# Performance work log

Measured on AMD Instinct MI355X. Metric: run time of the kernel, lower is better.

Reference implementation:

```python
import jax, jax.numpy as jnp
import numpy as np

N, K, G, E, OUT = 50000, 32, 512, 400000, 8
EPS = 1e-8


def setup_inputs() -> dict:
    key = jax.random.key(0)
    ks = jax.random.split(key, 9)
    X = jax.random.uniform(ks[0], (N, G), dtype=jnp.float32)          # counts-like, non-negative
    Mu = jax.random.uniform(ks[1], (K, G), dtype=jnp.float32)
    Var = jax.random.uniform(ks[2], (K, G), dtype=jnp.float32) + 0.5  # keep variances bounded away from 0
    edge_index = jax.random.randint(ks[3], (2, E), 0, N)
    # learned parameters
    W = jax.random.normal(ks[4], (N, K), dtype=jnp.float32) * 0.1     # module inits zeros; small randn for non-trivial grads
    S = jnp.ones((N, 1), jnp.float32)
    glorot = float(np.sqrt(6.0 / (G + OUT)))
    Wl = jax.random.uniform(ks[5], (G, OUT), jnp.float32, -glorot, glorot)
    bl = jnp.zeros((OUT,), jnp.float32)
    Wr = jax.random.uniform(ks[6], (G, OUT), jnp.float32, -glorot, glorot)
    br = jnp.zeros((OUT,), jnp.float32)
    att = jax.random.normal(ks[7], (OUT,), jnp.float32) * 0.3
    return dict(X=X, Mu=Mu, Var=Var, W=W, S=S, Wl=Wl, bl=bl, Wr=Wr, br=br, att=att, edge_index=edge_index)


def reference(X, Mu, Var, W, S, Wl, bl, Wr, br, att, edge_index):
    P = jax.nn.softmax(W, axis=1)                                     # [N,K]

    # Gaussian NLL term: F[n,k] = -0.5 * sum_g (X[n,g] - Mu[k,g]*S[n])^2 / Var[k,g]
    # expanded into three GEMM-shaped contractions to avoid the [N,K,G] intermediate
    inv_var = 1.0 / Var                                               # [K,G]
    q1 = (X * X) @ inv_var.T                                          # [N,K]
    q2 = X @ (Mu * inv_var).T                                         # [N,K]
    q3 = jnp.sum(Mu * Mu * inv_var, axis=1)                           # [K]
    s = S[:, 0]                                                       # [N]
    Fmat = -0.5 * (q1 - 2.0 * s[:, None] * q2 + (s * s)[:, None] * q3[None, :])
    ll_prot = jnp.sum(P * Fmat) / X.shape[0]

    # GATv2 attention (heads=1, out=8, no self loops): only alpha is consumed downstream
    src, dst = edge_index[0], edge_index[1]
    xl = X @ Wl + bl                                                  # source transform [N,8]
    xr = X @ Wr + br                                                  # target transform [N,8]
    e = jax.nn.leaky_relu(xl[src] + xr[dst], 0.2) @ att               # [E]
    # segment softmax over edges grouped by destination node
    m = jax.lax.stop_gradient(jax.ops.segment_max(e, dst, num_segments=N))
    ex = jnp.exp(e - m[dst])
    denom = jax.ops.segment_sum(ex, dst, num_segments=N)
    alpha = ex / denom[dst]                                           # [E]

    ce_space = -jnp.sum(P[src] * alpha[:, None] * jnp.log(P[dst] + EPS)) / X.shape[0]
    return ll_prot, ce_space, P
```

## Files before the change

### kernel.cpp

```cpp
#include <hip/hip_runtime.h>
#include <hip/hip_bf16.h>
#include <math.h>

#define N_NODES 50000
#define K_COMP  32
#define G_DIM   512
#define E_EDGES 400000
#define OUT_DIM 8
#define EPSV    1e-8f

#define NPB 16
#define NB_NODE (N_NODES / NPB)
#define NB_E1   ((E_EDGES + 255) / 256)
#define NB_CE   ((E_EDGES / 2 + 255) / 256)

typedef __attribute__((ext_vector_type(8))) short short8;
typedef __attribute__((ext_vector_type(8))) unsigned short ushort8;
typedef __attribute__((ext_vector_type(4))) unsigned short ushort4v;
typedef __attribute__((ext_vector_type(4))) float f32x4;

static const size_t OFF_T     = 0;
static const size_t OFF_Q3    = OFF_T + 80 * 512;
static const size_t OFF_XL    = OFF_Q3 + 64;
static const size_t OFF_XR    = OFF_XL + (size_t)N_NODES * 8;
static const size_t OFF_PC    = OFF_XR + (size_t)N_NODES * 8;
static const size_t OFF_LOGP  = OFF_PC + (size_t)N_NODES * 32;
static const size_t OFF_CON   = OFF_LOGP + (size_t)N_NODES * 32;
static const size_t OFF_DENOM = OFF_CON + E_EDGES;
static const size_t OFF_PLL   = OFF_DENOM + N_NODES;
static const size_t OFF_PCE   = OFF_PLL + 4096;

__device__ __forceinline__ unsigned short f2bf(float f) {
    __hip_bfloat16 h = __float2bfloat16(f);
    return *(unsigned short*)&h;
}
__device__ __forceinline__ float bf2f(unsigned short u) {
    unsigned v = ((unsigned)u) << 16;
    return __uint_as_float(v);
}

__global__ __launch_bounds__(256)
void prep_kernel(const float* __restrict__ Var, const float* __restrict__ Mu,
                 const float* __restrict__ Wl, const float* __restrict__ Wr,
                 unsigned short* __restrict__ Tb, float* __restrict__ denom,
                 float* __restrict__ q3) {
    int idx = blockIdx.x * 256 + threadIdx.x;
    if (idx < 80 * 512) {
        int r = idx >> 9;
        int g = idx & 511;
        float v;
        if (r < 32)      v = 1.0f / Var[r * 512 + g];
        else if (r < 64) { int k = r - 32; v = Mu[k * 512 + g] / Var[k * 512 + g]; }
        else if (r < 72) { int o = r - 64; v = Wl[g * 8 + o]; }
        else             { int o = r - 72; v = Wr[g * 8 + o]; }
        int dest = ((g >> 5) * 5 + (r >> 4)) * 512 + (r & 15) * 32 + (((g & 31) >> 3) << 3) + (g & 7);
        Tb[dest] = f2bf(v);
    }
    if (idx < N_NODES) denom[idx] = 0.0f;

    if (blockIdx.x < 32) {
        int k = blockIdx.x;
        int t = threadIdx.x;
        float s = 0.0f;
        for (int g = t; g < 512; g += 256) {
            float mu = Mu[k * 512 + g];
            s += mu * mu / Var[k * 512 + g];
        }
        for (int off = 32; off; off >>= 1) s += __shfl_down(s, off);
        __shared__ float sQ[4];
        if ((t & 63) == 0) sQ[t >> 6] = s;
        __syncthreads();
        if (t == 0) q3[k] = sQ[0] + sQ[1] + sQ[2] + sQ[3];
    }
}

__global__ __launch_bounds__(128, 5)
void node_kernel(const float* __restrict__ X, const float* __restrict__ W,
                 const float* __restrict__ S, const float* __restrict__ bl,
                 const float* __restrict__ br, const unsigned short* __restrict__ Tb,
                 const float* __restrict__ q3, float* __restrict__ outP,
                 unsigned short* __restrict__ Pcb, unsigned short* __restrict__ logPb,
                 float* __restrict__ xl, float* __restrict__ xr,
                 float* __restrict__ pll) {
    __shared__ float sAccH[2][NPB][81];
    __shared__ float sLL[2];

    const int t = threadIdx.x;
    const int lane = t & 63;
    const int wv = t >> 6;
    const int col = lane & 15;
    const int kg  = lane >> 4;

    const int node = blockIdx.x * NPB + col;
    const float* xrow = X + (size_t)node * 512 + wv * 256 + kg * 8;

    f32x4 acc[5];
#pragma unroll
    for (int i = 0; i < 5; ++i) acc[i] = (f32x4){0.f, 0.f, 0.f, 0.f};

    float4 v0 = *(const float4*)(xrow);
    float4 v1 = *(const float4*)(xrow + 4);

#pragma unroll
    for (int gc = 0; gc < 256; gc += 32) {
        float4 n0v, n1v;
        if (gc + 32 < 256) {
            n0v = *(const float4*)(xrow + gc + 32);
            n1v = *(const float4*)(xrow + gc + 36);
        }
        const unsigned short* bbase =
            Tb + (size_t)(wv * 8 + (gc >> 5)) * 5 * 512 + col * 32 + kg * 8;
        short8 b0 = *(const short8*)(bbase);
        short8 b1 = *(const short8*)(bbase + 512);
        short8 b2 = *(const short8*)(bbase + 1024);
        short8 b3 = *(const short8*)(bbase + 1536);
        short8 b4 = *(const short8*)(bbase + 2048);

        short8 ax, ax2;
        ax[0] = (short)f2bf(v0.x); ax[1] = (short)f2bf(v0.y);
        ax[2] = (short)f2bf(v0.z); ax[3] = (short)f2bf(v0.w);
        ax[4] = (short)f2bf(v1.x); ax[5] = (short)f2bf(v1.y);
        ax[6] = (short)f2bf(v1.z); ax[7] = (short)f2bf(v1.w);
        ax2[0] = (short)f2bf(v0.x * v0.x); ax2[1] = (short)f2bf(v0.y * v0.y);
        ax2[2] = (short)f2bf(v0.z * v0.z); ax2[3] = (short)f2bf(v0.w * v0.w);
        ax2[4] = (short)f2bf(v1.x * v1.x); ax2[5] = (short)f2bf(v1.y * v1.y);
        ax2[6] = (short)f2bf(v1.z * v1.z); ax2[7] = (short)f2bf(v1.w * v1.w);

        acc[0] = __builtin_amdgcn_mfma_f32_16x16x32_bf16(ax2, b0, acc[0], 0, 0, 0);
        acc[1] = __builtin_amdgcn_mfma_f32_16x16x32_bf16(ax2, b1, acc[1], 0, 0, 0);
        acc[2] = __builtin_amdgcn_mfma_f32_16x16x32_bf16(ax,  b2, acc[2], 0, 0, 0);
        acc[3] = __builtin_amdgcn_mfma_f32_16x16x32_bf16(ax,  b3, acc[3], 0, 0, 0);
        acc[4] = __builtin_amdgcn_mfma_f32_16x16x32_bf16(ax,  b4, acc[4], 0, 0, 0);

        v0 = n0v; v1 = n1v;
    }

#pragma unroll
    for (int tile = 0; tile < 5; ++tile)
#pragma unroll
        for (int r = 0; r < 4; ++r)
            sAccH[wv][kg * 4 + r][tile * 16 + col] = acc[tile][r];
    __syncthreads();

    const int nn = t >> 3;
    const int j = t & 7;
    const int n = blockIdx.x * NPB + nn;

    float sv = S[n];
    float sv2 = sv * sv;
    float4 wv4 = *(const float4*)(W + (size_t)n * 32 + j * 4);
    float w[4] = {wv4.x, wv4.y, wv4.z, wv4.w};
    float wm = fmaxf(fmaxf(w[0], w[1]), fmaxf(w[2], w[3]));
    wm = fmaxf(wm, __shfl_xor(wm, 1));
    wm = fmaxf(wm, __shfl_xor(wm, 2));
    wm = fmaxf(wm, __shfl_xor(wm, 4));
    float p[4], ps = 0.0f;
#pragma unroll
    for (int i = 0; i < 4; ++i) { p[i] = __expf(w[i] - wm); ps += p[i]; }
    ps += __shfl_xor(ps, 1);
    ps += __shfl_xor(ps, 2);
    ps += __shfl_xor(ps, 4);
    float inv = 1.0f / ps;

    float pv[4];
    ushort4v pb, lb;
    float ll = 0.0f;
#pragma unroll
    for (int i = 0; i < 4; ++i) {
        int k = j * 4 + i;
        float P_ = p[i] * inv;
        pv[i] = P_;
        pb[i] = f2bf(P_);
        lb[i] = f2bf(__logf(P_ + EPSV));
        float q1k = sAccH[0][nn][k] + sAccH[1][nn][k];
        float q2k = sAccH[0][nn][32 + k] + sAccH[1][nn][32 + k];
        float f = -0.5f * (q1k - 2.0f * sv * q2k + sv2 * q3[k]);
        ll = fmaf(P_, f, ll);
    }
    ll += __shfl_xor(ll, 1);
    ll += __shfl_xor(ll, 2);
    ll += __shfl_xor(ll, 4);
    float llacc = (j == 0) ? ll : 0.0f;

    size_t base = (size_t)n * 32 + j * 4;
    float2* op = (float2*)(outP + base);
    op[0] = make_float2(pv[0], pv[1]);
    op[1] = make_float2(pv[2], pv[3]);
    *(ushort4v*)&Pcb[base] = pb;
    *(ushort4v*)&logPb[base] = lb;

    float xlv = (sAccH[0][nn][64 + j] + sAccH[1][nn][64 + j]) + bl[j];
    float xrv = (sAccH[0][nn][72 + j] + sAccH[1][nn][72 + j]) + br[j];
    xl[(size_t)n * 8 + j] = xlv;
    xr[(size_t)n * 8 + j] = xrv;

    for (int off = 32; off; off >>= 1) llacc += __shfl_down(llacc, off);
    if ((t & 63) == 0) sLL[wv] = llacc;
    __syncthreads();
    if (t == 0) pll[blockIdx.x] = sLL[0] + sLL[1];
}

__global__ __launch_bounds__(256, 4)
void edge1_kernel(const int* __restrict__ ei, const float* __restrict__ xl,
                  const float* __restrict__ xr, const float* __restrict__ att,
                  const unsigned short* __restrict__ Pcb,
                  const unsigned short* __restrict__ logPb,
                  float* __restrict__ contrib, float* __restrict__ denom) {
    int i = blockIdx.x * 256 + threadIdx.x;
    if (i >= E_EDGES) return;
    int s = ei[i];
    int d = ei[E_EDGES + i];
    const float4* ap = (const float4*)(xl + (size_t)s * 8);
    const float4* bp = (const float4*)(xr + (size_t)d * 8);
    const ushort8* pp = (const ushort8*)&Pcb[(size_t)s * 32];
    const ushort8* lp = (const ushort8*)&logPb[(size_t)d * 32];
    float4 a0 = ap[0], a1 = ap[1];
    float4 b0 = bp[0], b1 = bp[1];
    ushort8 pa = pp[0], pb_ = pp[1], pc = pp[2], pd = pp[3];
    ushort8 la = lp[0], lb_ = lp[1], lc = lp[2], ld = lp[3];
    const float4* atp = (const float4*)att;
    float4 t0 = atp[0], t1 = atp[1];
    float at[8] = {t0.x, t0.y, t0.z, t0.w, t1.x, t1.y, t1.z, t1.w};
    float h[8] = {a0.x + b0.x, a0.y + b0.y, a0.z + b0.z, a0.w + b0.w,
                  a1.x + b1.x, a1.y + b1.y, a1.z + b1.z, a1.w + b1.w};
    float ev = 0.0f;
#pragma unroll
    for (int q = 0; q < 8; ++q) {
        float hv = h[q];
        hv = hv > 0.0f ? hv : 0.2f * hv;
        ev = fmaf(hv, at[q], ev);
    }
    float x = __expf(ev);
    atomicAdd(denom + d, x);

    float dot = 0.0f;
#pragma unroll
    for (int r = 0; r < 8; ++r) {
        dot = fmaf(bf2f(pa[r]),  bf2f(la[r]),  dot);
        dot = fmaf(bf2f(pb_[r]), bf2f(lb_[r]), dot);
        dot = fmaf(bf2f(pc[r]),  bf2f(lc[r]),  dot);
        dot = fmaf(bf2f(pd[r]),  bf2f(ld[r]),  dot);
    }
    contrib[i] = x * dot;
}

__global__ __launch_bounds__(256, 4)
void edge2_kernel(const int* __restrict__ ei, const float* __restrict__ contrib,
                  const float* __restrict__ denom, float* __restrict__ pce) {
    const int t = threadIdx.x;
    const int base = (blockIdx.x * 256 + t) * 2;
    float ce = 0.0f;
    if (base < E_EDGES) {
        int2 dd = *(const int2*)&ei[E_EDGES + base];
        float2 cv = *(const float2*)&contrib[base];
        float den0 = denom[dd.x];
        float den1 = denom[dd.y];
        ce = cv.x / den0 + cv.y / den1;
    }
    for (int off = 32; off; off >>= 1) ce += __shfl_down(ce, off);
    __shared__ float sC[4];
    if ((t & 63) == 0) sC[t >> 6] = ce;
    __syncthreads();
    if (t == 0) pce[blockIdx.x] = sC[0] + sC[1] + sC[2] + sC[3];
}

__global__ __launch_bounds__(256)
void finalize_kernel(const float* __restrict__ pll, const float* __restrict__ pce,
                     float* __restrict__ out) {
    const int t = threadIdx.x;
    float a = 0.0f, b = 0.0f;
    for (int i = t; i < NB_NODE; i += 256) a += pll[i];
    for (int i = t; i < NB_CE; i += 256) b += pce[i];
    for (int off = 32; off; off >>= 1) {
        a += __shfl_down(a, off);
        b += __shfl_down(b, off);
    }
    __shared__ float sA[4], sB[4];
    if ((t & 63) == 0) { sA[t >> 6] = a; sB[t >> 6] = b; }
    __syncthreads();
    if (t == 0) {
        float ll = sA[0] + sA[1] + sA[2] + sA[3];
        float ce = sB[0] + sB[1] + sB[2] + sB[3];
        out[0] = ll / (float)N_NODES;
        out[1] = -ce / (float)N_NODES;
    }
}

extern "C" void kernel_launch(void* const* d_in, const int* in_sizes, int n_in,
                              void* d_out, int out_size, void* d_ws, size_t ws_size,
                              hipStream_t stream) {
    const float* X   = (const float*)d_in[0];
    const float* Mu  = (const float*)d_in[1];
    const float* Var = (const float*)d_in[2];
    const float* W   = (const float*)d_in[3];
    const float* S   = (const float*)d_in[4];
    const float* Wl  = (const float*)d_in[5];
    const float* bl  = (const float*)d_in[6];
    const float* Wr  = (const float*)d_in[7];
    const float* br  = (const float*)d_in[8];
    const float* att = (const float*)d_in[9];
    const int*   ei  = (const int*)d_in[10];
    float* out = (float*)d_out;
    float* ws  = (float*)d_ws;

    unsigned short* Tb      = (unsigned short*)(ws + OFF_T);
    float*          q3      = ws + OFF_Q3;
    float*          xl      = ws + OFF_XL;
    float*          xr      = ws + OFF_XR;
    unsigned short* Pcb     = (unsigned short*)(ws + OFF_PC);
    unsigned short* logPb   = (unsigned short*)(ws + OFF_LOGP);
    float*          contrib = ws + OFF_CON;
    float*          denom   = ws + OFF_DENOM;
    float*          pll     = ws + OFF_PLL;
    float*          pce     = ws + OFF_PCE;

    prep_kernel<<<(N_NODES + 255) / 256, 256, 0, stream>>>(Var, Mu, Wl, Wr, Tb, denom, q3);
    node_kernel<<<NB_NODE, 128, 0, stream>>>(X, W, S, bl, br, Tb, q3,
                                             out + 2, Pcb, logPb, xl, xr, pll);
    edge1_kernel<<<NB_E1, 256, 0, stream>>>(ei, xl, xr, att, Pcb, logPb, contrib, denom);
    edge2_kernel<<<NB_CE, 256, 0, stream>>>(ei, contrib, denom, pce);
    finalize_kernel<<<1, 256, 0, stream>>>(pll, pce, out);
}
```

Before: 80.94 us.

## Fold edge softmax normalization into per-destination atomics and pack node records

Because alpha normalizes by a per-destination denominator, the CE sum can be taken per destination as sum(x*dot)/sum(x). The edge kernel now atomically accumulates both quantities per node, and a small per-node kernel replaces the second pass over all edges and the per-edge contrib buffer. Per-node xl plus P and xr plus logP are also packed into contiguous 128-byte source and destination records, so each edge gathers one record per endpoint. The cost is a second atomic per edge and a larger zero-init in prep.

```diff
diff --git a/kernel.cpp b/kernel.cpp
--- a/kernel.cpp
+++ b/kernel.cpp
@@ -12,23 +12,21 @@
 #define NPB 16
 #define NB_NODE (N_NODES / NPB)
 #define NB_E1   ((E_EDGES + 255) / 256)
-#define NB_CE   ((E_EDGES / 2 + 255) / 256)
+#define NB_CEN  ((N_NODES + 255) / 256)
+#define NB_PREP ((2 * N_NODES + 255) / 256)
 
 typedef __attribute__((ext_vector_type(8))) short short8;
 typedef __attribute__((ext_vector_type(8))) unsigned short ushort8;
 typedef __attribute__((ext_vector_type(4))) unsigned short ushort4v;
 typedef __attribute__((ext_vector_type(4))) float f32x4;
 
-static const size_t OFF_T     = 0;
-static const size_t OFF_Q3    = OFF_T + 80 * 512;
-static const size_t OFF_XL    = OFF_Q3 + 64;
-static const size_t OFF_XR    = OFF_XL + (size_t)N_NODES * 8;
-static const size_t OFF_PC    = OFF_XR + (size_t)N_NODES * 8;
-static const size_t OFF_LOGP  = OFF_PC + (size_t)N_NODES * 32;
-static const size_t OFF_CON   = OFF_LOGP + (size_t)N_NODES * 32;
-static const size_t OFF_DENOM = OFF_CON + E_EDGES;
-static const size_t OFF_PLL   = OFF_DENOM + N_NODES;
-static const size_t OFF_PCE   = OFF_PLL + 4096;
+static const size_t OFF_T    = 0;
+static const size_t OFF_Q3   = OFF_T + 80 * 512;
+static const size_t OFF_SRC  = OFF_Q3 + 64;
+static const size_t OFF_DST  = OFF_SRC + (size_t)N_NODES * 32;
+static const size_t OFF_ND   = OFF_DST + (size_t)N_NODES * 32;
+static const size_t OFF_PLL  = OFF_ND + 2 * (size_t)N_NODES;
+static const size_t OFF_PCE  = OFF_PLL + 4096;
 
 __device__ __forceinline__ unsigned short f2bf(float f) {
     __hip_bfloat16 h = __float2bfloat16(f);
@@ -42,7 +40,7 @@
 __global__ __launch_bounds__(256)
 void prep_kernel(const float* __restrict__ Var, const float* __restrict__ Mu,
                  const float* __restrict__ Wl, const float* __restrict__ Wr,
-                 unsigned short* __restrict__ Tb, float* __restrict__ denom,
+                 unsigned short* __restrict__ Tb, float* __restrict__ nd,
                  float* __restrict__ q3) {
     int idx = blockIdx.x * 256 + threadIdx.x;
     if (idx < 80 * 512) {
@@ -56,7 +54,7 @@
         int dest = ((g >> 5) * 5 + (r >> 4)) * 512 + (r & 15) * 32 + (((g & 31) >> 3) << 3) + (g & 7);
         Tb[dest] = f2bf(v);
     }
-    if (idx < N_NODES) denom[idx] = 0.0f;
+    if (idx < 2 * N_NODES) nd[idx] = 0.0f;
 
     if (blockIdx.x < 32) {
         int k = blockIdx.x;
@@ -79,8 +77,7 @@
                  const float* __restrict__ S, const float* __restrict__ bl,
                  const float* __restrict__ br, const unsigned short* __restrict__ Tb,
                  const float* __restrict__ q3, float* __restrict__ outP,
-                 unsigned short* __restrict__ Pcb, unsigned short* __restrict__ logPb,
-                 float* __restrict__ xl, float* __restrict__ xr,
+                 float* __restrict__ srcRec, float* __restrict__ dstRec,
                  float* __restrict__ pll) {
     __shared__ float sAccH[2][NPB][81];
     __shared__ float sLL[2];
@@ -186,13 +183,13 @@
     float2* op = (float2*)(outP + base);
     op[0] = make_float2(pv[0], pv[1]);
     op[1] = make_float2(pv[2], pv[3]);
-    *(ushort4v*)&Pcb[base] = pb;
-    *(ushort4v*)&logPb[base] = lb;
-
-    float xlv = (sAccH[0][nn][64 + j] + sAccH[1][nn][64 + j]) + bl[j];
-    float xrv = (sAccH[0][nn][72 + j] + sAccH[1][nn][72 + j]) + br[j];
-    xl[(size_t)n * 8 + j] = xlv;
-    xr[(size_t)n * 8 + j] = xrv;
+
+    float* sr = srcRec + (size_t)n * 32;
+    float* dr = dstRec + (size_t)n * 32;
+    *(ushort4v*)&((unsigned short*)sr)[16 + j * 4] = pb;
+    *(ushort4v*)&((unsigned short*)dr)[16 + j * 4] = lb;
+    sr[j] = (sAccH[0][nn][64 + j] + sAccH[1][nn][64 + j]) + bl[j];
+    dr[j] = (sAccH[0][nn][72 + j] + sAccH[1][nn][72 + j]) + br[j];
 
     for (int off = 32; off; off >>= 1) llacc += __shfl_down(llacc, off);
     if ((t & 63) == 0) sLL[wv] = llacc;
@@ -201,21 +198,19 @@
 }
 
 __global__ __launch_bounds__(256, 4)
-void edge1_kernel(const int* __restrict__ ei, const float* __restrict__ xl,
-                  const float* __restrict__ xr, const float* __restrict__ att,
-                  const unsigned short* __restrict__ Pcb,
-                  const unsigned short* __restrict__ logPb,
-                  float* __restrict__ contrib, float* __restrict__ denom) {
+void edge1_kernel(const int* __restrict__ ei, const float* __restrict__ srcRec,
+                  const float* __restrict__ dstRec, const float* __restrict__ att,
+                  float* __restrict__ nd) {
     int i = blockIdx.x * 256 + threadIdx.x;
     if (i >= E_EDGES) return;
     int s = ei[i];
     int d = ei[E_EDGES + i];
-    const float4* ap = (const float4*)(xl + (size_t)s * 8);
-    const float4* bp = (const float4*)(xr + (size_t)d * 8);
-    const ushort8* pp = (const ushort8*)&Pcb[(size_t)s * 32];
-    const ushort8* lp = (const ushort8*)&logPb[(size_t)d * 32];
-    float4 a0 = ap[0], a1 = ap[1];
-    float4 b0 = bp[0], b1 = bp[1];
+    const float4* sp = (const float4*)(srcRec + (size_t)s * 32);
+    const float4* dp = (const float4*)(dstRec + (size_t)d * 32);
+    float4 a0 = sp[0], a1 = sp[1];
+    float4 b0 = dp[0], b1 = dp[1];
+    const ushort8* pp = (const ushort8*)(sp + 2);
+    const ushort8* lp = (const ushort8*)(dp + 2);
     ushort8 pa = pp[0], pb_ = pp[1], pc = pp[2], pd = pp[3];
     ushort8 la = lp[0], lb_ = lp[1], lc = lp[2], ld = lp[3];
     const float4* atp = (const float4*)att;
@@ -231,7 +226,6 @@
         ev = fmaf(hv, at[q], ev);
     }
     float x = __expf(ev);
-    atomicAdd(denom + d, x);
 
     float dot = 0.0f;
 #pragma unroll
@@ -241,21 +235,18 @@
         dot = fmaf(bf2f(pc[r]),  bf2f(lc[r]),  dot);
         dot = fmaf(bf2f(pd[r]),  bf2f(ld[r]),  dot);
     }
-    contrib[i] = x * dot;
-}
-
-__global__ __launch_bounds__(256, 4)
-void edge2_kernel(const int* __restrict__ ei, const float* __restrict__ contrib,
-                  const float* __restrict__ denom, float* __restrict__ pce) {
+    atomicAdd(&nd[2 * d],     x);
+    atomicAdd(&nd[2 * d + 1], x * dot);
+}
+
+__global__ __launch_bounds__(256)
+void ce_node_kernel(const float* __restrict__ nd, float* __restrict__ pce) {
     const int t = threadIdx.x;
-    const int base = (blockIdx.x * 256 + t) * 2;
+    int i = blockIdx.x * 256 + t;
     float ce = 0.0f;
-    if (base < E_EDGES) {
-        int2 dd = *(const int2*)&ei[E_EDGES + base];
-        float2 cv = *(const float2*)&contrib[base];
-        float den0 = denom[dd.x];
-        float den1 = denom[dd.y];
-        ce = cv.x / den0 + cv.y / den1;
+    if (i < N_NODES) {
+        float2 v = *(const float2*)&nd[2 * i];
+        if (v.x > 0.0f) ce = v.y / v.x;
     }
     for (int off = 32; off; off >>= 1) ce += __shfl_down(ce, off);
     __shared__ float sC[4];
@@ -270,7 +261,7 @@
     const int t = threadIdx.x;
     float a = 0.0f, b = 0.0f;
     for (int i = t; i < NB_NODE; i += 256) a += pll[i];
-    for (int i = t; i < NB_CE; i += 256) b += pce[i];
+    for (int i = t; i < NB_CEN; i += 256) b += pce[i];
     for (int off = 32; off; off >>= 1) {
         a += __shfl_down(a, off);
         b += __shfl_down(b, off);
@@ -303,21 +294,18 @@
     float* out = (float*)d_out;
     float* ws  = (float*)d_ws;
 
-    unsigned short* Tb      = (unsigned short*)(ws + OFF_T);
-    float*          q3      = ws + OFF_Q3;
-    float*          xl      = ws + OFF_XL;
-    float*          xr      = ws + OFF_XR;
-    unsigned short* Pcb     = (unsigned short*)(ws + OFF_PC);
-    unsigned short* logPb   = (unsigned short*)(ws + OFF_LOGP);
-    float*          contrib = ws + OFF_CON;
-    float*          denom   = ws + OFF_DENOM;
-    float*          pll     = ws + OFF_PLL;
-    float*          pce     = ws + OFF_PCE;
-
-    prep_kernel<<<(N_NODES + 255) / 256, 256, 0, stream>>>(Var, Mu, Wl, Wr, Tb, denom, q3);
+    unsigned short* Tb     = (unsigned short*)(ws + OFF_T);
+    float*          q3     = ws + OFF_Q3;
+    float*          srcRec = ws + OFF_SRC;
+    float*          dstRec = ws + OFF_DST;
+    float*          nd     = ws + OFF_ND;
+    float*          pll    = ws + OFF_PLL;
+    float*          pce    = ws + OFF_PCE;
+
+    prep_kernel<<<NB_PREP, 256, 0, stream>>>(Var, Mu, Wl, Wr, Tb, nd, q3);
     node_kernel<<<NB_NODE, 128, 0, stream>>>(X, W, S, bl, br, Tb, q3,
-                                             out + 2, Pcb, logPb, xl, xr, pll);
-    edge1_kernel<<<NB_E1, 256, 0, stream>>>(ei, xl, xr, att, Pcb, logPb, contrib, denom);
-    edge2_kernel<<<NB_CE, 256, 0, stream>>>(ei, contrib, denom, pce);
+                                             out + 2, srcRec, dstRec, pll);
+    edge1_kernel<<<NB_E1, 256, 0, stream>>>(ei, srcRec, dstRec, att, nd);
+    ce_node_kernel<<<NB_CEN, 256, 0, stream>>>(nd, pce);
     finalize_kernel<<<1, 256, 0, stream>>>(pll, pce, out);
 }
```

Measured after the change: 95.75 us. 18.3% more time.
